# Kernel tuning notes

Measured on AMD Instinct MI355X. Metric: run time of the kernel, lower is better.

## Reference

```python
import jax, jax.numpy as jnp
import numpy as np

D_MODEL = 1024
N_HEAD = 16
D_K = D_MODEL // N_HEAD
NEG = -1e9


def setup_inputs() -> dict:
    key = jax.random.key(0)
    ks = jax.random.split(key, 9)
    B, S = 2, 2048
    scale = 1.0 / np.sqrt(D_MODEL)
    x = jax.random.normal(ks[0], (B, S, D_MODEL), dtype=jnp.float32)
    mask = jnp.tril(jnp.ones((S, S), dtype=jnp.int32))  # causal: 0 => masked
    Wq = jax.random.normal(ks[1], (D_MODEL, D_MODEL), dtype=jnp.float32) * scale
    bq = jnp.zeros((D_MODEL,), dtype=jnp.float32)
    Wk = jax.random.normal(ks[2], (D_MODEL, D_MODEL), dtype=jnp.float32) * scale
    bk = jnp.zeros((D_MODEL,), dtype=jnp.float32)
    Wv = jax.random.normal(ks[3], (D_MODEL, D_MODEL), dtype=jnp.float32) * scale
    bv = jnp.zeros((D_MODEL,), dtype=jnp.float32)
    Wo = jax.random.normal(ks[4], (D_MODEL, D_MODEL), dtype=jnp.float32) * scale
    bo = jnp.zeros((D_MODEL,), dtype=jnp.float32)
    return {"x": x, "mask": mask, "Wq": Wq, "bq": bq, "Wk": Wk, "bk": bk,
            "Wv": Wv, "bv": bv, "Wo": Wo, "bo": bo}


def reference(x, mask, Wq, bq, Wk, bk, Wv, bv, Wo, bo):
    B, S, _ = x.shape
    # torch Linear: y = x @ W.T + b
    def split_heads(y):  # [B,S,D] -> [B,H,S,d_k]
        return y.reshape(B, S, N_HEAD, D_K).transpose(0, 2, 1, 3)
    Q = split_heads(x @ Wq.T + bq)
    K = split_heads(x @ Wk.T + bk)
    V = split_heads(x @ Wv.T + bv)
    scores = jnp.einsum('bhqd,bhkd->bhqk', Q, K) / jnp.sqrt(jnp.float32(D_K))
    scores = jnp.where(mask[None, None, :, :] == 0, jnp.float32(NEG), scores)
    attn = jax.nn.softmax(scores, axis=-1)
    out = jnp.einsum('bhqk,bhkd->bhqd', attn, V)
    out = out.transpose(0, 2, 1, 3).reshape(B, S, D_MODEL)
    return out @ Wo.T + bo
```

## Files before the change

### kernel.cpp

```cpp
#include <hip/hip_runtime.h>
#include <hip/hip_bf16.h>
#include <stdint.h>

#define DM    1024
#define NHEAD 16
#define DKH   64
#define SEQ   2048
#define NB    2
#define MTOT  (NB*SEQ)
#define LSTR  72
#define QSCL  0.18033688f

typedef __hip_bfloat16 bf16;
typedef __attribute__((ext_vector_type(8))) short bf16x8;
typedef __attribute__((ext_vector_type(4))) short bf16x4;
typedef __attribute__((ext_vector_type(4))) float f32x4;

#define MFMA16(a,b,c) __builtin_amdgcn_mfma_f32_16x16x32_bf16((a),(b),(c),0,0,0)

#if __has_builtin(__builtin_amdgcn_exp2f)
#define EXP2F(x) __builtin_amdgcn_exp2f(x)
#else
#define EXP2F(x) __expf(0.69314718056f * (x))
#endif

__device__ __forceinline__ void async_copy16(const void* g, void* l) {
  __builtin_amdgcn_global_load_lds((const __attribute__((address_space(1))) uint32_t*)g,
                                   (__attribute__((address_space(3))) uint32_t*)l,
                                   16, 0, 0);
}

__device__ __forceinline__ short f32_bf16_bits(float f) {
  uint32_t u = __builtin_bit_cast(uint32_t, f);
  u += 0x7FFFu + ((u >> 16) & 1u);
  return (short)(u >> 16);
}

__global__ __launch_bounds__(256) void k_cvt_all(
    const float* __restrict__ x,  const float* __restrict__ Wq,
    const float* __restrict__ Wk, const float* __restrict__ Wv,
    const float* __restrict__ Wo,
    bf16* __restrict__ xb,  bf16* __restrict__ Wqb, bf16* __restrict__ Wkb,
    bf16* __restrict__ Wvb, bf16* __restrict__ Wob) {
  const int NX = (MTOT*DM)/4;
  const int NW = (DM*DM)/4;
  int i = blockIdx.x * 256 + threadIdx.x;
  const float* s; bf16* d; int j; float scl = 1.0f;
  if (i < NX) { s = x; d = xb; j = i; }
  else {
    int t = i - NX;
    int k = t >> 18;
    j = t & (NW - 1);
    s = (k == 0) ? Wq : (k == 1) ? Wk : (k == 2) ? Wv : Wo;
    d = (k == 0) ? Wqb : (k == 1) ? Wkb : (k == 2) ? Wvb : Wob;
    if (k == 0) scl = QSCL;
  }
  float4 v = ((const float4*)s)[j];
  bf16x4 o;
  o[0] = f32_bf16_bits(v.x * scl);
  o[1] = f32_bf16_bits(v.y * scl);
  o[2] = f32_bf16_bits(v.z * scl);
  o[3] = f32_bf16_bits(v.w * scl);
  ((bf16x4*)d)[j] = o;
}

__global__ __launch_bounds__(256) void k_gemm_qkv(
    const bf16* __restrict__ x,
    const bf16* __restrict__ Wq, const bf16* __restrict__ Wk, const bf16* __restrict__ Wv,
    const float* __restrict__ bq, const float* __restrict__ bk, const float* __restrict__ bv,
    bf16* __restrict__ Q, bf16* __restrict__ K, bf16* __restrict__ V) {
  const bf16* W; const float* bias; bf16* C; float bs;
  if (blockIdx.z == 0)      { W = Wq; bias = bq; C = Q; bs = QSCL; }
  else if (blockIdx.z == 1) { W = Wk; bias = bk; C = K; bs = 1.0f; }
  else                      { W = Wv; bias = bv; C = V; bs = 1.0f; }

  __shared__ __align__(16) short As[128*32];
  __shared__ __align__(16) short Bs[128*32];
  const int tid  = threadIdx.x;
  const int lane = tid & 63;
  const int w    = tid >> 6;
  const int wm   = (w & 1) << 6;
  const int wn   = (w >> 1) << 6;
  const int bm   = blockIdx.x << 7;
  const int bn   = blockIdx.y << 7;
  const int m16  = lane & 15;
  const int quad = lane >> 4;
  const int koff = quad << 3;
  const int c0   = (w << 7) | lane;

  f32x4 acc[4][4] = {};

  for (int k0 = 0; k0 < DM; k0 += 32) {
    __syncthreads();
#pragma unroll
    for (int it = 0; it < 2; ++it) {
      int c   = c0 + (it << 6);
      int row = c >> 2;
      int kc  = c & 3;
      async_copy16(x + (size_t)(bm + row) * DM + k0 + (kc << 3),
                   &As[(size_t)((w << 7) + (it << 6)) << 3]);
      async_copy16(W + (size_t)(bn + row) * DM + k0 + (kc << 3),
                   &Bs[(size_t)((w << 7) + (it << 6)) << 3]);
    }
    __syncthreads();

    bf16x8 af[4], bfv[4];
#pragma unroll
    for (int t = 0; t < 4; ++t)
      af[t]  = *(const bf16x8*)&As[(wm + t*16 + m16) * 32 + koff];
#pragma unroll
    for (int t = 0; t < 4; ++t)
      bfv[t] = *(const bf16x8*)&Bs[(wn + t*16 + m16) * 32 + koff];
#pragma unroll
    for (int i = 0; i < 4; ++i)
#pragma unroll
      for (int j = 0; j < 4; ++j)
        acc[i][j] = MFMA16(af[i], bfv[j], acc[i][j]);
  }

  const int crow0 = bm + wm + (quad << 2);
  const int ccol0 = bn + wn + m16;
#pragma unroll
  for (int j = 0; j < 4; ++j) {
    float bv = bias[ccol0 + j*16] * bs;
#pragma unroll
    for (int i = 0; i < 4; ++i)
#pragma unroll
      for (int r = 0; r < 4; ++r)
        C[(size_t)(crow0 + i*16 + r) * DM + ccol0 + j*16] =
            (bf16)(acc[i][j][r] + bv);
  }
}

__global__ __launch_bounds__(256) void k_gemm_o(
    const bf16* __restrict__ A, const bf16* __restrict__ W,
    const float* __restrict__ bias, float* __restrict__ C) {
  __shared__ __align__(16) short As[128*32];
  __shared__ __align__(16) short Bs[64*32];
  const int tid  = threadIdx.x;
  const int lane = tid & 63;
  const int w    = tid >> 6;
  const int wm   = (w & 1) << 6;
  const int wn   = (w >> 1) << 5;
  const int bm   = blockIdx.x << 7;
  const int bn   = blockIdx.y << 6;
  const int m16  = lane & 15;
  const int quad = lane >> 4;
  const int koff = quad << 3;
  const int cA   = (w << 7) | lane;
  const int cB   = (w << 6) | lane;

  f32x4 acc[4][2] = {};

  for (int k0 = 0; k0 < DM; k0 += 32) {
    __syncthreads();
#pragma unroll
    for (int it = 0; it < 2; ++it) {
      int c   = cA + (it << 6);
      int row = c >> 2;
      int kc  = c & 3;
      async_copy16(A + (size_t)(bm + row) * DM + k0 + (kc << 3),
                   &As[(size_t)((w << 7) + (it << 6)) << 3]);
    }
    {
      int row = cB >> 2;
      int kc  = cB & 3;
      async_copy16(W + (size_t)(bn + row) * DM + k0 + (kc << 3),
                   &Bs[(size_t)(w << 6) << 3]);
    }
    __syncthreads();

    bf16x8 af[4], bfv[2];
#pragma unroll
    for (int t = 0; t < 4; ++t)
      af[t]  = *(const bf16x8*)&As[(wm + t*16 + m16) * 32 + koff];
#pragma unroll
    for (int t = 0; t < 2; ++t)
      bfv[t] = *(const bf16x8*)&Bs[(wn + t*16 + m16) * 32 + koff];
#pragma unroll
    for (int i = 0; i < 4; ++i)
#pragma unroll
      for (int j = 0; j < 2; ++j)
        acc[i][j] = MFMA16(af[i], bfv[j], acc[i][j]);
  }

  const int crow0 = bm + wm + (quad << 2);
  const int ccol0 = bn + wn + m16;
#pragma unroll
  for (int j = 0; j < 2; ++j) {
    float bv = bias[ccol0 + j*16];
#pragma unroll
    for (int i = 0; i < 4; ++i)
#pragma unroll
      for (int r = 0; r < 4; ++r)
        C[(size_t)(crow0 + i*16 + r) * DM + ccol0 + j*16] =
            acc[i][j][r] + bv;
  }
}

__global__ __launch_bounds__(256) void k_transpose_v(const bf16* __restrict__ V,
                                                     bf16* __restrict__ Vt) {
  __shared__ __align__(16) short tile[64][LSTR];
  const int tid = threadIdx.x;
  const int s0  = blockIdx.x << 6;
  const int bh  = blockIdx.y;
  const int b   = bh >> 4, h = bh & 15;
#pragma unroll
  for (int it = 0; it < 2; ++it) {
    int c = tid + (it << 8);
    int s = c >> 3, dc = c & 7;
    bf16x8 v = *(const bf16x8*)&V[(size_t)(b*SEQ + s0 + s) * DM + h*DKH + (dc << 3)];
    *(bf16x8*)&tile[s][dc << 3] = v;
  }
  __syncthreads();
#pragma unroll
  for (int it = 0; it < 2; ++it) {
    int c = tid + (it << 8);
    int d = c >> 3, sc = c & 7;
    bf16x8 ov;
#pragma unroll
    for (int i = 0; i < 8; ++i) {
      int p = (sc << 3) + i;
      ov[i] = tile[(p & 3) * 16 + (p >> 2)][d];
    }
    *(bf16x8*)&Vt[((size_t)bh * DKH + d) * SEQ + s0 + (sc << 3)] = ov;
  }
}

__global__ __launch_bounds__(256) void k_attn(const bf16* __restrict__ Q,
                                              const bf16* __restrict__ K,
                                              const bf16* __restrict__ Vt,
                                              bf16* __restrict__ ctx) {
  __shared__ __align__(16) short Ks[64*LSTR];
  __shared__ __align__(16) short Vs[64*LSTR];
  __shared__ __align__(16) short Ps[4][16*LSTR];

  const int tid  = threadIdx.x;
  const int lane = tid & 63;
  const int w    = tid >> 6;
  const int pi   = blockIdx.x;
  const int bh   = blockIdx.y;
  const int b    = bh >> 4, h = bh & 15;
  const int m16  = lane & 15, quad = lane >> 4;
  const int koff = quad << 3;

  const int qt        = (w < 2) ? pi : 63 - pi;
  const int qw        = (qt << 5) + ((w & 1) << 4);
  const int my_ktmax  = qt >> 1;
  const int blk_ktmax = (63 - pi) >> 1;

  const int r0 = tid >> 3, r1 = r0 + 32, c0 = (tid & 7) << 3;

  const bf16* Kb  = K  + (size_t)(b*SEQ) * DM + h*DKH;
  const bf16* Vtb = Vt + (size_t)bh * DKH * SEQ;

  const bf16* Qb = Q + (size_t)(b*SEQ + qw) * DM + h*DKH;
  bf16x8 qf0 = *(const bf16x8*)(Qb + (size_t)m16*DM + koff);
  bf16x8 qf1 = *(const bf16x8*)(Qb + (size_t)m16*DM + 32 + koff);

  f32x4 o[4] = {};
  float ps[4] = {0.f, 0.f, 0.f, 0.f};
  short* Pw = Ps[w];
  const int qg = qw + (quad << 2);

  bf16x8 pk0 = *(const bf16x8*)(Kb  + (size_t)r0*DM + c0);
  bf16x8 pk1 = *(const bf16x8*)(Kb  + (size_t)r1*DM + c0);
  bf16x8 pv0 = *(const bf16x8*)(Vtb + (size_t)r0*SEQ + c0);
  bf16x8 pv1 = *(const bf16x8*)(Vtb + (size_t)r1*SEQ + c0);

  for (int kt = 0; kt <= blk_ktmax; ++kt) {
    __syncthreads();
    *(bf16x8*)&Ks[r0*LSTR + c0] = pk0;
    *(bf16x8*)&Ks[r1*LSTR + c0] = pk1;
    *(bf16x8*)&Vs[r0*LSTR + c0] = pv0;
    *(bf16x8*)&Vs[r1*LSTR + c0] = pv1;
    __syncthreads();

    if (kt < blk_ktmax) {
      const int kn = (kt + 1) << 6;
      pk0 = *(const bf16x8*)(Kb  + (size_t)(kn + r0)*DM + c0);
      pk1 = *(const bf16x8*)(Kb  + (size_t)(kn + r1)*DM + c0);
      pv0 = *(const bf16x8*)(Vtb + (size_t)r0*SEQ + kn + c0);
      pv1 = *(const bf16x8*)(Vtb + (size_t)r1*SEQ + kn + c0);
    }

    if (kt <= my_ktmax) {
      f32x4 sc[4];
#pragma unroll
      for (int st = 0; st < 4; ++st) {
        bf16x8 kf0 = *(const bf16x8*)&Ks[(st*16 + m16)*LSTR + koff];
        bf16x8 kf1 = *(const bf16x8*)&Ks[(st*16 + m16)*LSTR + 32 + koff];
        f32x4 a = {};
        a = MFMA16(qf0, kf0, a);
        a = MFMA16(qf1, kf1, a);
        sc[st] = a;
      }
      const int kk0 = kt << 6;
      if (kt == my_ktmax) {
#pragma unroll
        for (int r = 0; r < 4; ++r) {
          float e[4];
#pragma unroll
          for (int st = 0; st < 4; ++st) {
            float t = EXP2F(sc[st][r]);
            t = (kk0 + st*16 + m16 <= qg + r) ? t : 0.f;
            e[st] = t; ps[r] += t;
          }
          uint32_t lo = (uint16_t)f32_bf16_bits(e[0]) |
                        ((uint32_t)(uint16_t)f32_bf16_bits(e[1]) << 16);
          uint32_t hi = (uint16_t)f32_bf16_bits(e[2]) |
                        ((uint32_t)(uint16_t)f32_bf16_bits(e[3]) << 16);
          *(uint64_t*)&Pw[((quad << 2) + r)*LSTR + (m16 << 2)] =
              (uint64_t)lo | ((uint64_t)hi << 32);
        }
      } else {
#pragma unroll
        for (int r = 0; r < 4; ++r) {
          float e[4];
#pragma unroll
          for (int st = 0; st < 4; ++st) {
            float t = EXP2F(sc[st][r]);
            e[st] = t; ps[r] += t;
          }
          uint32_t lo = (uint16_t)f32_bf16_bits(e[0]) |
                        ((uint32_t)(uint16_t)f32_bf16_bits(e[1]) << 16);
          uint32_t hi = (uint16_t)f32_bf16_bits(e[2]) |
                        ((uint32_t)(uint16_t)f32_bf16_bits(e[3]) << 16);
          *(uint64_t*)&Pw[((quad << 2) + r)*LSTR + (m16 << 2)] =
              (uint64_t)lo | ((uint64_t)hi << 32);
        }
      }
      asm volatile("s_waitcnt lgkmcnt(0)" ::: "memory");
      bf16x8 pa0 = *(const bf16x8*)&Pw[m16*LSTR + koff];
      bf16x8 pa1 = *(const bf16x8*)&Pw[m16*LSTR + 32 + koff];
#pragma unroll
      for (int t = 0; t < 4; ++t) {
        bf16x8 vf0 = *(const bf16x8*)&Vs[(t*16 + m16)*LSTR + koff];
        bf16x8 vf1 = *(const bf16x8*)&Vs[(t*16 + m16)*LSTR + 32 + koff];
        o[t] = MFMA16(pa0, vf0, o[t]);
        o[t] = MFMA16(pa1, vf1, o[t]);
      }
    }
  }

  bf16* Cb = ctx + (size_t)(b*SEQ + qw) * DM + h*DKH;
#pragma unroll
  for (int r = 0; r < 4; ++r) {
    float v = ps[r];
    v += __shfl_xor(v, 1, 64);
    v += __shfl_xor(v, 2, 64);
    v += __shfl_xor(v, 4, 64);
    v += __shfl_xor(v, 8, 64);
    float inv = 1.0f / v;
#pragma unroll
    for (int t = 0; t < 4; ++t)
      Cb[(size_t)((quad << 2) + r) * DM + t*16 + m16] = (bf16)(o[t][r] * inv);
  }
}

extern "C" void kernel_launch(void* const* d_in, const int* in_sizes, int n_in,
                              void* d_out, int out_size, void* d_ws, size_t ws_size,
                              hipStream_t stream) {
  const float* x  = (const float*)d_in[0];
  const float* Wq = (const float*)d_in[2];
  const float* bq = (const float*)d_in[3];
  const float* Wk = (const float*)d_in[4];
  const float* bk = (const float*)d_in[5];
  const float* Wv = (const float*)d_in[6];
  const float* bv = (const float*)d_in[7];
  const float* Wo = (const float*)d_in[8];
  const float* bo = (const float*)d_in[9];
  float* out = (float*)d_out;

  const size_t SZ = (size_t)MTOT * DM;
  const size_t WZ = (size_t)DM * DM;
  bf16* xb  = (bf16*)d_ws;
  bf16* Wqb = xb  + SZ;
  bf16* Wkb = Wqb + WZ;
  bf16* Wvb = Wkb + WZ;
  bf16* Wob = Wvb + WZ;
  bf16* Qb  = Wob + WZ;
  bf16* Kb  = Qb  + SZ;
  bf16* Vb  = Kb  + SZ;
  bf16* Vtb = Vb  + SZ;
  bf16* Cx  = xb;

  k_cvt_all<<<(SZ/4 + 4*(WZ/4))/256, 256, 0, stream>>>(
      x, Wq, Wk, Wv, Wo, xb, Wqb, Wkb, Wvb, Wob);

  k_gemm_qkv<<<dim3(MTOT/128, DM/128, 3), 256, 0, stream>>>(
      xb, Wqb, Wkb, Wvb, bq, bk, bv, Qb, Kb, Vb);
  k_transpose_v<<<dim3(SEQ/64, NB*NHEAD), 256, 0, stream>>>(Vb, Vtb);
  k_attn<<<dim3(32, NB*NHEAD), 256, 0, stream>>>(Qb, Kb, Vtb, Cx);
  k_gemm_o<<<dim3(MTOT/128, DM/64), 256, 0, stream>>>(Cx, Wob, bo, out);
}
```

Before: 203.3 us.

## Remap GEMM and attention blocks per XCD and split attention into smaller blocks

Both GEMM kernels now remap their block IDs so that consecutive blocks dispatched to the same XCD share M-tiles and reuse data in that XCD's L2. The attention kernel is restructured from 256-thread blocks that paired a short and a long query tile into 128-thread blocks, each handling one 32-row query tile. These blocks are launched longest-first and grouped by head per XCD, with a launch-bounds occupancy hint. The change is meant to improve L2 locality and load balance and to remove the idle warps of the paired-tile scheme. In exchange it launches twice as many blocks and loads K/V tiles with fewer threads per block.

```diff
diff --git a/kernel.cpp b/kernel.cpp
--- a/kernel.cpp
+++ b/kernel.cpp
@@ -69,10 +69,18 @@
     const bf16* __restrict__ Wq, const bf16* __restrict__ Wk, const bf16* __restrict__ Wv,
     const float* __restrict__ bq, const float* __restrict__ bk, const float* __restrict__ bv,
     bf16* __restrict__ Q, bf16* __restrict__ K, bf16* __restrict__ V) {
+  const int id  = blockIdx.x + (blockIdx.y << 5) + (blockIdx.z << 8);
+  const int xcd = id & 7;
+  const int jj  = id >> 3;
+  const int bxi = (xcd << 2) | (jj & 3);
+  const int rem = jj >> 2;
+  const int byi = rem & 7;
+  const int bzi = rem >> 3;
+
   const bf16* W; const float* bias; bf16* C; float bs;
-  if (blockIdx.z == 0)      { W = Wq; bias = bq; C = Q; bs = QSCL; }
-  else if (blockIdx.z == 1) { W = Wk; bias = bk; C = K; bs = 1.0f; }
-  else                      { W = Wv; bias = bv; C = V; bs = 1.0f; }
+  if (bzi == 0)      { W = Wq; bias = bq; C = Q; bs = QSCL; }
+  else if (bzi == 1) { W = Wk; bias = bk; C = K; bs = 1.0f; }
+  else               { W = Wv; bias = bv; C = V; bs = 1.0f; }
 
   __shared__ __align__(16) short As[128*32];
   __shared__ __align__(16) short Bs[128*32];
@@ -81,8 +89,8 @@
   const int w    = tid >> 6;
   const int wm   = (w & 1) << 6;
   const int wn   = (w >> 1) << 6;
-  const int bm   = blockIdx.x << 7;
-  const int bn   = blockIdx.y << 7;
+  const int bm   = bxi << 7;
+  const int bn   = byi << 7;
   const int m16  = lane & 15;
   const int quad = lane >> 4;
   const int koff = quad << 3;
@@ -135,6 +143,12 @@
 __global__ __launch_bounds__(256) void k_gemm_o(
     const bf16* __restrict__ A, const bf16* __restrict__ W,
     const float* __restrict__ bias, float* __restrict__ C) {
+  const int id  = blockIdx.x + (blockIdx.y << 5);
+  const int xcd = id & 7;
+  const int jj  = id >> 3;
+  const int bxi = (xcd << 2) | (jj & 3);
+  const int byi = jj >> 2;
+
   __shared__ __align__(16) short As[128*32];
   __shared__ __align__(16) short Bs[64*32];
   const int tid  = threadIdx.x;
@@ -142,8 +156,8 @@
   const int w    = tid >> 6;
   const int wm   = (w & 1) << 6;
   const int wn   = (w >> 1) << 5;
-  const int bm   = blockIdx.x << 7;
-  const int bn   = blockIdx.y << 6;
+  const int bm   = bxi << 7;
+  const int bn   = byi << 6;
   const int m16  = lane & 15;
   const int quad = lane >> 4;
   const int koff = quad << 3;
@@ -227,29 +241,32 @@
   }
 }
 
-__global__ __launch_bounds__(256) void k_attn(const bf16* __restrict__ Q,
-                                              const bf16* __restrict__ K,
-                                              const bf16* __restrict__ Vt,
-                                              bf16* __restrict__ ctx) {
+__global__ __launch_bounds__(128, 4) void k_attn(const bf16* __restrict__ Q,
+                                                 const bf16* __restrict__ K,
+                                                 const bf16* __restrict__ Vt,
+                                                 bf16* __restrict__ ctx) {
   __shared__ __align__(16) short Ks[64*LSTR];
   __shared__ __align__(16) short Vs[64*LSTR];
-  __shared__ __align__(16) short Ps[4][16*LSTR];
+  __shared__ __align__(16) short Ps[2][16*LSTR];
 
   const int tid  = threadIdx.x;
   const int lane = tid & 63;
   const int w    = tid >> 6;
-  const int pi   = blockIdx.x;
-  const int bh   = blockIdx.y;
+
+  const int id   = blockIdx.x + (blockIdx.y << 6);
+  const int xcd  = id & 7;
+  const int jj   = id >> 3;
+  const int bh   = (xcd << 2) | (jj >> 6);
+  const int qt   = 63 - (jj & 63);
   const int b    = bh >> 4, h = bh & 15;
+
   const int m16  = lane & 15, quad = lane >> 4;
   const int koff = quad << 3;
-
-  const int qt        = (w < 2) ? pi : 63 - pi;
-  const int qw        = (qt << 5) + ((w & 1) << 4);
-  const int my_ktmax  = qt >> 1;
-  const int blk_ktmax = (63 - pi) >> 1;
-
-  const int r0 = tid >> 3, r1 = r0 + 32, c0 = (tid & 7) << 3;
+  const int qw   = (qt << 5) + (w << 4);
+  const int ktmax = qt >> 1;
+
+  const int rs = tid >> 3;
+  const int cs = (tid & 7) << 3;
 
   const bf16* Kb  = K  + (size_t)(b*SEQ) * DM + h*DKH;
   const bf16* Vtb = Vt + (size_t)bh * DKH * SEQ;
@@ -263,28 +280,32 @@
   short* Pw = Ps[w];
   const int qg = qw + (quad << 2);
 
-  bf16x8 pk0 = *(const bf16x8*)(Kb  + (size_t)r0*DM + c0);
-  bf16x8 pk1 = *(const bf16x8*)(Kb  + (size_t)r1*DM + c0);
-  bf16x8 pv0 = *(const bf16x8*)(Vtb + (size_t)r0*SEQ + c0);
-  bf16x8 pv1 = *(const bf16x8*)(Vtb + (size_t)r1*SEQ + c0);
-
-  for (int kt = 0; kt <= blk_ktmax; ++kt) {
-    __syncthreads();
-    *(bf16x8*)&Ks[r0*LSTR + c0] = pk0;
-    *(bf16x8*)&Ks[r1*LSTR + c0] = pk1;
-    *(bf16x8*)&Vs[r0*LSTR + c0] = pv0;
-    *(bf16x8*)&Vs[r1*LSTR + c0] = pv1;
-    __syncthreads();
-
-    if (kt < blk_ktmax) {
+  bf16x8 pk[4], pv[4];
+#pragma unroll
+  for (int it = 0; it < 4; ++it) {
+    pk[it] = *(const bf16x8*)(Kb  + (size_t)(rs + 16*it)*DM  + cs);
+    pv[it] = *(const bf16x8*)(Vtb + (size_t)(rs + 16*it)*SEQ + cs);
+  }
+
+  for (int kt = 0; kt <= ktmax; ++kt) {
+    __syncthreads();
+#pragma unroll
+    for (int it = 0; it < 4; ++it) {
+      *(bf16x8*)&Ks[(rs + 16*it)*LSTR + cs] = pk[it];
+      *(bf16x8*)&Vs[(rs + 16*it)*LSTR + cs] = pv[it];
+    }
+    __syncthreads();
+
+    if (kt < ktmax) {
       const int kn = (kt + 1) << 6;
-      pk0 = *(const bf16x8*)(Kb  + (size_t)(kn + r0)*DM + c0);
-      pk1 = *(const bf16x8*)(Kb  + (size_t)(kn + r1)*DM + c0);
-      pv0 = *(const bf16x8*)(Vtb + (size_t)r0*SEQ + kn + c0);
-      pv1 = *(const bf16x8*)(Vtb + (size_t)r1*SEQ + kn + c0);
-    }
-
-    if (kt <= my_ktmax) {
+#pragma unroll
+      for (int it = 0; it < 4; ++it) {
+        pk[it] = *(const bf16x8*)(Kb  + (size_t)(kn + rs + 16*it)*DM + cs);
+        pv[it] = *(const bf16x8*)(Vtb + (size_t)(rs + 16*it)*SEQ + kn + cs);
+      }
+    }
+
+    {
       f32x4 sc[4];
 #pragma unroll
       for (int st = 0; st < 4; ++st) {
@@ -296,7 +317,7 @@
         sc[st] = a;
       }
       const int kk0 = kt << 6;
-      if (kt == my_ktmax) {
+      if (kt == ktmax) {
 #pragma unroll
         for (int r = 0; r < 4; ++r) {
           float e[4];
@@ -391,6 +412,6 @@
   k_gemm_qkv<<<dim3(MTOT/128, DM/128, 3), 256, 0, stream>>>(
       xb, Wqb, Wkb, Wvb, bq, bk, bv, Qb, Kb, Vb);
   k_transpose_v<<<dim3(SEQ/64, NB*NHEAD), 256, 0, stream>>>(Vb, Vtb);
-  k_attn<<<dim3(32, NB*NHEAD), 256, 0, stream>>>(Qb, Kb, Vtb, Cx);
+  k_attn<<<dim3(64, NB*NHEAD*2), 128, 0, stream>>>(Qb, Kb, Vtb, Cx);
   k_gemm_o<<<dim3(MTOT/128, DM/64), 256, 0, stream>>>(Cx, Wob, bo, out);
 }
```

New measurement: 247.1 us. 1.22x slower.
